# Optimization experiments

Hardware: AMD Instinct MI355X
Metric: run time of the kernel (lower is better)

## Reference

```python
import jax, jax.numpy as jnp
import numpy as np

B, T, C = 4, 4096, 1024


def setup_inputs() -> dict:
    key = jax.random.key(0)
    k_x, k_f, k_g, k_p = jax.random.split(key, 4)
    scale = 1.0 / np.sqrt(C)  # keep gate pre-activations well-scaled
    return {
        "x": jax.random.normal(k_x, (B, T, C), dtype=jnp.float32),
        "W_f_x": jax.random.normal(k_f, (C, C), dtype=jnp.float32) * scale,
        "W_g_x": jax.random.normal(k_g, (C, C), dtype=jnp.float32) * scale,
        "W_proj": jax.random.normal(k_p, (C, C), dtype=jnp.float32) * scale,
    }


def _cfc_scan(a, b):
    """Solve h_t = a_t * h_{t-1} + b_t with h_{-1}=0 along axis 1 (T).

    Associative op on linear maps: (A_l,B_l) then (A_r,B_r) composes to
    (A_r*A_l, A_r*B_l + B_r). With h_init=0, h_t = B-component.
    """
    def op(l, r):
        al, bl = l
        ar, br = r
        return ar * al, ar * bl + br
    _, h = jax.lax.associative_scan(op, (a, b), axis=1)
    return h


def reference(x, W_f_x, W_g_x, W_proj):
    # Gates depend on x only (parallel mode). nn.Linear: x @ W.T
    f = jax.nn.sigmoid(jnp.einsum("btc,dc->btd", x, W_f_x))  # (B,T,C)
    g = jnp.tanh(jnp.einsum("btc,dc->btd", x, W_g_x))        # (B,T,C)
    h = _cfc_scan(f, (1.0 - f) * g)                           # (B,T,C)
    return jnp.einsum("btc,dc->btd", h, W_proj)               # c_proj
```

## Files before the change

kernel.cpp:

```cpp
#include <hip/hip_runtime.h>
#include <hip/hip_bf16.h>
#include <stdint.h>

#define TT 4096
#define BB 4
#define CC 1024
#define MM (BB * TT)
#define NCHUNK 64
#define CHUNK_T (TT / NCHUNK)
#define NCHAIN (BB * CC)

typedef float f32x4 __attribute__((ext_vector_type(4)));
typedef __bf16 bf16x8 __attribute__((ext_vector_type(8)));

__device__ __forceinline__ float b2f(ushort u) {
  union { float f; uint32_t v; } x; x.v = ((uint32_t)u) << 16; return x.f;
}
__device__ __forceinline__ ushort f2b(float f) {
  union { float f; uint32_t u; } x; x.f = f;
  uint32_t r = x.u + 0x7fffu + ((x.u >> 16) & 1u);
  return (ushort)(r >> 16);
}

__device__ __forceinline__ void async_copy16(const ushort* g, ushort* l) {
  __builtin_amdgcn_global_load_lds(
      (__attribute__((address_space(1))) void*)(g),
      (__attribute__((address_space(3))) void*)(l), 16, 0, 0);
}

__global__ __launch_bounds__(256) void cvt_f32_bf16(const float* __restrict__ s,
                                                    ushort* __restrict__ d, int n4) {
  int i = blockIdx.x * 256 + threadIdx.x;
  if (i >= n4) return;
  float4 v = ((const float4*)s)[i];
  ushort4 o;
  o.x = f2b(v.x); o.y = f2b(v.y); o.z = f2b(v.z); o.w = f2b(v.w);
  ((ushort4*)d)[i] = o;
}

template <int MODE>
__global__ __launch_bounds__(256) void gemm_bt(const ushort* __restrict__ A,
                                               const ushort* __restrict__ Bw,
                                               float* __restrict__ outF,
                                               ushort* __restrict__ outB, int N) {
  constexpr int K = CC;
  __shared__ __align__(16) ushort sA[128 * 32];
  __shared__ __align__(16) ushort sB[128 * 32];
  const int tid = threadIdx.x;
  const int lane = tid & 63;
  const int wid = tid >> 6;
  const int wm = wid >> 1, wn = wid & 1;
  const long m0 = (long)blockIdx.y * 128;
  const long n0 = (long)blockIdx.x * 128;

  f32x4 acc[4][4];
#pragma unroll
  for (int i = 0; i < 4; ++i)
#pragma unroll
    for (int j = 0; j < 4; ++j) acc[i][j] = (f32x4){0.f, 0.f, 0.f, 0.f};

  const int srow = lane >> 2;
  const int scol = (lane & 3) * 8;
  const ushort* Ab = A + (m0 + srow) * K + scol;
  const ushort* Bb = Bw + (n0 + srow) * K + scol;

  for (int k0 = 0; k0 < K; k0 += 32) {
#pragma unroll
    for (int half = 0; half < 2; ++half) {
      const int ch = wid + half * 4;
      async_copy16(Ab + (long)ch * 16 * K + k0, &sA[ch * 512 + lane * 8]);
      async_copy16(Bb + (long)ch * 16 * K + k0, &sB[ch * 512 + lane * 8]);
    }
    __syncthreads();

    const int kq = lane >> 4;
    bf16x8 af[4], bfr[4];
#pragma unroll
    for (int i = 0; i < 4; ++i) {
      af[i]  = *(const bf16x8*)&sA[(wm * 64 + i * 16 + (lane & 15)) * 32 + kq * 8];
      bfr[i] = *(const bf16x8*)&sB[(wn * 64 + i * 16 + (lane & 15)) * 32 + kq * 8];
    }
#pragma unroll
    for (int i = 0; i < 4; ++i)
#pragma unroll
      for (int j = 0; j < 4; ++j)
        acc[i][j] = __builtin_amdgcn_mfma_f32_16x16x32_bf16(af[i], bfr[j], acc[i][j], 0, 0, 0);
    __syncthreads();
  }

  const int col = lane & 15;
  const int rq = lane >> 4;
#pragma unroll
  for (int i = 0; i < 4; ++i) {
#pragma unroll
    for (int j = 0; j < 4; ++j) {
      const long n = n0 + wn * 64 + j * 16 + col;
#pragma unroll
      for (int r = 0; r < 4; ++r) {
        const long m = m0 + wm * 64 + i * 16 + rq * 4 + r;
        float v = acc[i][j][r];
        if (MODE == 0) {
          outF[m * N + n] = v;
        } else {
          float act;
          if (n < CC) {
            act = 1.f / (1.f + __expf(-v));
          } else {
            float e = __expf(2.f * v);
            act = (e - 1.f) / (e + 1.f);
          }
          outB[m * (long)N + n] = f2b(act);
        }
      }
    }
  }
}

__global__ __launch_bounds__(256) void scan_pass1(const ushort* __restrict__ P,
                                                  float* __restrict__ cA,
                                                  float* __restrict__ cB) {
  const int chain = blockIdx.x * 256 + threadIdx.x;
  const int chunk = blockIdx.y;
  const int b = chain >> 10, c = chain & (CC - 1);
  const ushort* p = P + (size_t)(b * TT + chunk * CHUNK_T) * (2 * CC) + c;
  float A = 1.f, h = 0.f;
#pragma unroll 4
  for (int i = 0; i < CHUNK_T; ++i) {
    const float f = b2f(p[0]);
    const float g = b2f(p[CC]);
    p += 2 * CC;
    A *= f;
    h = fmaf(f, h, (1.f - f) * g);
  }
  cA[chunk * NCHAIN + chain] = A;
  cB[chunk * NCHAIN + chain] = h;
}

__global__ __launch_bounds__(256) void scan_pass2(const float* __restrict__ cA,
                                                  const float* __restrict__ cB,
                                                  float* __restrict__ hinit) {
  const int chain = blockIdx.x * 256 + threadIdx.x;
  float h = 0.f;
  for (int j = 0; j < NCHUNK; ++j) {
    hinit[j * NCHAIN + chain] = h;
    h = fmaf(cA[j * NCHAIN + chain], h, cB[j * NCHAIN + chain]);
  }
}

__global__ __launch_bounds__(256) void scan_pass3(const ushort* __restrict__ P,
                                                  const float* __restrict__ hinit,
                                                  ushort* __restrict__ H) {
  const int chain = blockIdx.x * 256 + threadIdx.x;
  const int chunk = blockIdx.y;
  const int b = chain >> 10, c = chain & (CC - 1);
  const ushort* p = P + (size_t)(b * TT + chunk * CHUNK_T) * (2 * CC) + c;
  ushort* hp = H + (size_t)(b * TT + chunk * CHUNK_T) * CC + c;
  float h = hinit[chunk * NCHAIN + chain];
#pragma unroll 4
  for (int i = 0; i < CHUNK_T; ++i) {
    const float f = b2f(p[0]);
    const float g = b2f(p[CC]);
    p += 2 * CC;
    h = fmaf(f, h, (1.f - f) * g);
    *hp = f2b(h);
    hp += CC;
  }
}

extern "C" void kernel_launch(void* const* d_in, const int* in_sizes, int n_in,
                              void* d_out, int out_size, void* d_ws, size_t ws_size,
                              hipStream_t stream) {
  const float* x  = (const float*)d_in[0];
  const float* Wf = (const float*)d_in[1];
  const float* Wg = (const float*)d_in[2];
  const float* Wp = (const float*)d_in[3];

  char* ws = (char*)d_ws;
  ushort* xb   = (ushort*)(ws);
  ushort* Hb   = xb;
  ushort* Wcat = (ushort*)(ws + 33554432);
  ushort* Wpb  = (ushort*)(ws + 33554432 + 4194304);
  ushort* P    = (ushort*)(ws + 33554432 + 4194304 + 2097152);
  char* tail   = ws + 33554432 + 4194304 + 2097152 + 67108864;
  float* cA    = (float*)(tail);
  float* cB    = (float*)(tail + 1048576);
  float* hinit = (float*)(tail + 2097152);
  (void)ws_size; (void)in_sizes; (void)n_in; (void)out_size;

  cvt_f32_bf16<<<MM * CC / 4 / 256, 256, 0, stream>>>(x, xb, MM * CC / 4);
  cvt_f32_bf16<<<CC * CC / 4 / 256, 256, 0, stream>>>(Wf, Wcat, CC * CC / 4);
  cvt_f32_bf16<<<CC * CC / 4 / 256, 256, 0, stream>>>(Wg, Wcat + CC * CC, CC * CC / 4);
  cvt_f32_bf16<<<CC * CC / 4 / 256, 256, 0, stream>>>(Wp, Wpb, CC * CC / 4);

  dim3 g1(2 * CC / 128, MM / 128);
  gemm_bt<1><<<g1, 256, 0, stream>>>(xb, Wcat, nullptr, P, 2 * CC);

  dim3 gs(NCHAIN / 256, NCHUNK);
  scan_pass1<<<gs, 256, 0, stream>>>(P, cA, cB);
  scan_pass2<<<NCHAIN / 256, 256, 0, stream>>>(cA, cB, hinit);
  scan_pass3<<<gs, 256, 0, stream>>>(P, hinit, Hb);

  dim3 g3(CC / 128, MM / 128);
  gemm_bt<0><<<g3, 256, 0, stream>>>(Hb, Wpb, (float*)d_out, nullptr, CC);
}
```

Measured before the change: 316.2 us.

## Fuse conversions, swizzle GEMM LDS, fold scan pass2 into pass3, narrow output tiles

After: 324.3 us. 2.6% more time.

```diff
diff --git a/kernel.cpp b/kernel.cpp
--- a/kernel.cpp
+++ b/kernel.cpp
@@ -28,62 +28,74 @@
       (__attribute__((address_space(3))) void*)(l), 16, 0, 0);
 }
 
-__global__ __launch_bounds__(256) void cvt_f32_bf16(const float* __restrict__ s,
-                                                    ushort* __restrict__ d, int n4) {
-  int i = blockIdx.x * 256 + threadIdx.x;
-  if (i >= n4) return;
-  float4 v = ((const float4*)s)[i];
+__global__ __launch_bounds__(256) void cvt_all(const float* __restrict__ x,
+                                               const float* __restrict__ wf,
+                                               const float* __restrict__ wg,
+                                               const float* __restrict__ wp,
+                                               ushort* __restrict__ xb,
+                                               ushort* __restrict__ wcat,
+                                               ushort* __restrict__ wpb) {
+  const int i = blockIdx.x * 256 + threadIdx.x;
+  const float* s; ushort* d; int off;
+  if (i < 4194304)            { s = x;  d = xb;              off = i; }
+  else if (i < 4456448)       { s = wf; d = wcat;            off = i - 4194304; }
+  else if (i < 4718592)       { s = wg; d = wcat + 1048576;  off = i - 4456448; }
+  else                        { s = wp; d = wpb;             off = i - 4718592; }
+  float4 v = ((const float4*)s)[off];
   ushort4 o;
   o.x = f2b(v.x); o.y = f2b(v.y); o.z = f2b(v.z); o.w = f2b(v.w);
-  ((ushort4*)d)[i] = o;
-}
-
-template <int MODE>
+  ((ushort4*)d)[off] = o;
+}
+
+template <int TN, int WTN, int MODE>
 __global__ __launch_bounds__(256) void gemm_bt(const ushort* __restrict__ A,
                                                const ushort* __restrict__ Bw,
                                                float* __restrict__ outF,
                                                ushort* __restrict__ outB, int N) {
   constexpr int K = CC;
+  constexpr int JN = WTN / 16;
+  constexpr int NCH = (128 + TN) / 16;
   __shared__ __align__(16) ushort sA[128 * 32];
-  __shared__ __align__(16) ushort sB[128 * 32];
+  __shared__ __align__(16) ushort sB[TN * 32];
   const int tid = threadIdx.x;
   const int lane = tid & 63;
   const int wid = tid >> 6;
   const int wm = wid >> 1, wn = wid & 1;
   const long m0 = (long)blockIdx.y * 128;
-  const long n0 = (long)blockIdx.x * 128;
-
-  f32x4 acc[4][4];
+  const long n0 = (long)blockIdx.x * TN;
+
+  f32x4 acc[4][JN];
 #pragma unroll
   for (int i = 0; i < 4; ++i)
 #pragma unroll
-    for (int j = 0; j < 4; ++j) acc[i][j] = (f32x4){0.f, 0.f, 0.f, 0.f};
+    for (int j = 0; j < JN; ++j) acc[i][j] = (f32x4){0.f, 0.f, 0.f, 0.f};
 
   const int srow = lane >> 2;
-  const int scol = (lane & 3) * 8;
-  const ushort* Ab = A + (m0 + srow) * K + scol;
-  const ushort* Bb = Bw + (n0 + srow) * K + scol;
+  const int kcf = (lane & 3) ^ ((lane >> 3) & 3);
+  const ushort* Ab = A + (m0 + srow) * K + kcf * 8;
+  const ushort* Bb = Bw + (n0 + srow) * K + kcf * 8;
+  const int slot = (lane >> 4) ^ ((lane >> 1) & 3);
+  const int rlo = lane & 15;
 
   for (int k0 = 0; k0 < K; k0 += 32) {
 #pragma unroll
-    for (int half = 0; half < 2; ++half) {
-      const int ch = wid + half * 4;
-      async_copy16(Ab + (long)ch * 16 * K + k0, &sA[ch * 512 + lane * 8]);
-      async_copy16(Bb + (long)ch * 16 * K + k0, &sB[ch * 512 + lane * 8]);
+    for (int ch = wid; ch < NCH; ch += 4) {
+      if (ch < 8) async_copy16(Ab + (long)ch * 16 * K + k0, &sA[ch * 512 + lane * 8]);
+      else async_copy16(Bb + (long)(ch - 8) * 16 * K + k0, &sB[(ch - 8) * 512 + lane * 8]);
     }
     __syncthreads();
 
-    const int kq = lane >> 4;
-    bf16x8 af[4], bfr[4];
-#pragma unroll
-    for (int i = 0; i < 4; ++i) {
-      af[i]  = *(const bf16x8*)&sA[(wm * 64 + i * 16 + (lane & 15)) * 32 + kq * 8];
-      bfr[i] = *(const bf16x8*)&sB[(wn * 64 + i * 16 + (lane & 15)) * 32 + kq * 8];
-    }
+    bf16x8 af[4], bfr[JN];
 #pragma unroll
     for (int i = 0; i < 4; ++i)
-#pragma unroll
-      for (int j = 0; j < 4; ++j)
+      af[i] = *(const bf16x8*)&sA[(wm * 64 + i * 16 + rlo) * 32 + slot * 8];
+#pragma unroll
+    for (int j = 0; j < JN; ++j)
+      bfr[j] = *(const bf16x8*)&sB[(wn * WTN + j * 16 + rlo) * 32 + slot * 8];
+#pragma unroll
+    for (int i = 0; i < 4; ++i)
+#pragma unroll
+      for (int j = 0; j < JN; ++j)
         acc[i][j] = __builtin_amdgcn_mfma_f32_16x16x32_bf16(af[i], bfr[j], acc[i][j], 0, 0, 0);
     __syncthreads();
   }
@@ -93,8 +105,8 @@
 #pragma unroll
   for (int i = 0; i < 4; ++i) {
 #pragma unroll
-    for (int j = 0; j < 4; ++j) {
-      const long n = n0 + wn * 64 + j * 16 + col;
+    for (int j = 0; j < JN; ++j) {
+      const long n = n0 + wn * WTN + j * 16 + col;
 #pragma unroll
       for (int r = 0; r < 4; ++r) {
         const long m = m0 + wm * 64 + i * 16 + rq * 4 + r;
@@ -119,51 +131,56 @@
 __global__ __launch_bounds__(256) void scan_pass1(const ushort* __restrict__ P,
                                                   float* __restrict__ cA,
                                                   float* __restrict__ cB) {
-  const int chain = blockIdx.x * 256 + threadIdx.x;
+  const int pc = blockIdx.x * 256 + threadIdx.x;
   const int chunk = blockIdx.y;
-  const int b = chain >> 10, c = chain & (CC - 1);
-  const ushort* p = P + (size_t)(b * TT + chunk * CHUNK_T) * (2 * CC) + c;
-  float A = 1.f, h = 0.f;
+  const int b = pc >> 9, c2 = (pc & 511) * 2;
+  const ushort2* p =
+      (const ushort2*)(P + (size_t)(b * TT + chunk * CHUNK_T) * (2 * CC) + c2);
+  float A0 = 1.f, A1 = 1.f, h0 = 0.f, h1 = 0.f;
 #pragma unroll 4
   for (int i = 0; i < CHUNK_T; ++i) {
-    const float f = b2f(p[0]);
-    const float g = b2f(p[CC]);
-    p += 2 * CC;
-    A *= f;
-    h = fmaf(f, h, (1.f - f) * g);
-  }
-  cA[chunk * NCHAIN + chain] = A;
-  cB[chunk * NCHAIN + chain] = h;
-}
-
-__global__ __launch_bounds__(256) void scan_pass2(const float* __restrict__ cA,
+    const ushort2 fu = p[0];
+    const ushort2 gu = p[CC / 2];
+    p += CC;
+    const float f0 = b2f(fu.x), f1 = b2f(fu.y);
+    const float g0 = b2f(gu.x), g1 = b2f(gu.y);
+    A0 *= f0; A1 *= f1;
+    h0 = fmaf(f0, h0, (1.f - f0) * g0);
+    h1 = fmaf(f1, h1, (1.f - f1) * g1);
+  }
+  ((float2*)(cA + chunk * NCHAIN + b * CC))[c2 >> 1] = (float2){A0, A1};
+  ((float2*)(cB + chunk * NCHAIN + b * CC))[c2 >> 1] = (float2){h0, h1};
+}
+
+__global__ __launch_bounds__(256) void scan_pass3(const ushort* __restrict__ P,
+                                                  const float* __restrict__ cA,
                                                   const float* __restrict__ cB,
-                                                  float* __restrict__ hinit) {
-  const int chain = blockIdx.x * 256 + threadIdx.x;
-  float h = 0.f;
-  for (int j = 0; j < NCHUNK; ++j) {
-    hinit[j * NCHAIN + chain] = h;
-    h = fmaf(cA[j * NCHAIN + chain], h, cB[j * NCHAIN + chain]);
-  }
-}
-
-__global__ __launch_bounds__(256) void scan_pass3(const ushort* __restrict__ P,
-                                                  const float* __restrict__ hinit,
                                                   ushort* __restrict__ H) {
-  const int chain = blockIdx.x * 256 + threadIdx.x;
+  const int pc = blockIdx.x * 256 + threadIdx.x;
   const int chunk = blockIdx.y;
-  const int b = chain >> 10, c = chain & (CC - 1);
-  const ushort* p = P + (size_t)(b * TT + chunk * CHUNK_T) * (2 * CC) + c;
-  ushort* hp = H + (size_t)(b * TT + chunk * CHUNK_T) * CC + c;
-  float h = hinit[chunk * NCHAIN + chain];
+  const int b = pc >> 9, c2 = (pc & 511) * 2;
+  const int ci = b * CC + c2;
+  float h0 = 0.f, h1 = 0.f;
+  for (int j = 0; j < chunk; ++j) {
+    const float2 a = *(const float2*)(cA + j * NCHAIN + ci);
+    const float2 bb = *(const float2*)(cB + j * NCHAIN + ci);
+    h0 = fmaf(a.x, h0, bb.x);
+    h1 = fmaf(a.y, h1, bb.y);
+  }
+  const ushort2* p =
+      (const ushort2*)(P + (size_t)(b * TT + chunk * CHUNK_T) * (2 * CC) + c2);
+  ushort2* hp = (ushort2*)(H + (size_t)(b * TT + chunk * CHUNK_T) * CC + c2);
 #pragma unroll 4
   for (int i = 0; i < CHUNK_T; ++i) {
-    const float f = b2f(p[0]);
-    const float g = b2f(p[CC]);
-    p += 2 * CC;
-    h = fmaf(f, h, (1.f - f) * g);
-    *hp = f2b(h);
-    hp += CC;
+    const ushort2 fu = p[0];
+    const ushort2 gu = p[CC / 2];
+    p += CC;
+    const float f0 = b2f(fu.x), f1 = b2f(fu.y);
+    const float g0 = b2f(gu.x), g1 = b2f(gu.y);
+    h0 = fmaf(f0, h0, (1.f - f0) * g0);
+    h1 = fmaf(f1, h1, (1.f - f1) * g1);
+    *hp = (ushort2){f2b(h0), f2b(h1)};
+    hp += CC / 2;
   }
 }
 
@@ -184,22 +201,17 @@
   char* tail   = ws + 33554432 + 4194304 + 2097152 + 67108864;
   float* cA    = (float*)(tail);
   float* cB    = (float*)(tail + 1048576);
-  float* hinit = (float*)(tail + 2097152);
   (void)ws_size; (void)in_sizes; (void)n_in; (void)out_size;
 
-  cvt_f32_bf16<<<MM * CC / 4 / 256, 256, 0, stream>>>(x, xb, MM * CC / 4);
-  cvt_f32_bf16<<<CC * CC / 4 / 256, 256, 0, stream>>>(Wf, Wcat, CC * CC / 4);
-  cvt_f32_bf16<<<CC * CC / 4 / 256, 256, 0, stream>>>(Wg, Wcat + CC * CC, CC * CC / 4);
-  cvt_f32_bf16<<<CC * CC / 4 / 256, 256, 0, stream>>>(Wp, Wpb, CC * CC / 4);
+  cvt_all<<<19456, 256, 0, stream>>>(x, Wf, Wg, Wp, xb, Wcat, Wpb);
 
   dim3 g1(2 * CC / 128, MM / 128);
-  gemm_bt<1><<<g1, 256, 0, stream>>>(xb, Wcat, nullptr, P, 2 * CC);
-
-  dim3 gs(NCHAIN / 256, NCHUNK);
+  gemm_bt<128, 64, 1><<<g1, 256, 0, stream>>>(xb, Wcat, nullptr, P, 2 * CC);
+
+  dim3 gs(NCHAIN / 2 / 256, NCHUNK);
   scan_pass1<<<gs, 256, 0, stream>>>(P, cA, cB);
-  scan_pass2<<<NCHAIN / 256, 256, 0, stream>>>(cA, cB, hinit);
-  scan_pass3<<<gs, 256, 0, stream>>>(P, hinit, Hb);
-
-  dim3 g3(CC / 128, MM / 128);
-  gemm_bt<0><<<g3, 256, 0, stream>>>(Hb, Wpb, (float*)d_out, nullptr, CC);
-}
+  scan_pass3<<<gs, 256, 0, stream>>>(P, cA, cB, Hb);
+
+  dim3 g3(CC / 64, MM / 128);
+  gemm_bt<64, 32, 0><<<g3, 256, 0, stream>>>(Hb, Wpb, (float*)d_out, nullptr, CC);
+}
```
